# Kernel optimization log

Measured on AMD Instinct MI355X. Metric: run time of the kernel, lower is better.

Reference implementation:

```python
import jax, jax.numpy as jnp
import numpy as np

N_NODES = 10000
N_EDGES = 320000
N_GRAPHS = 64
D_IN = 256
D_HID = 256
D_OUT = 16


def sage_conv(x, edge_index, w_l, b_l, w_r):
    # PyG SAGEConv: out = lin_l(mean_{j in N(i)} x_j) + lin_r(x_i)
    src, dst = edge_index[0], edge_index[1]
    msg = x[src]                                   # [E, d] gather
    summed = jax.ops.segment_sum(msg, dst, num_segments=x.shape[0])
    ones = jnp.ones((edge_index.shape[1],), dtype=x.dtype)
    cnt = jax.ops.segment_sum(ones, dst, num_segments=x.shape[0])
    aggr = summed / jnp.maximum(cnt, 1.0)[:, None]  # mean aggregation
    return aggr @ w_l.T + b_l + x @ w_r.T


def setup_inputs() -> dict:
    key = jax.random.key(0)
    ks = jax.random.split(key, 12)

    def glorot(k, shape):
        lim = float(np.sqrt(6.0 / (shape[0] + shape[1])))
        return jax.random.uniform(k, shape, jnp.float32, -lim, lim)

    x = jax.random.normal(ks[0], (N_NODES, D_IN), jnp.float32)
    edge_index = jax.random.randint(ks[1], (2, N_EDGES), 0, N_NODES, jnp.int64)
    batch = jnp.sort(jax.random.randint(ks[2], (N_NODES,), 0, N_GRAPHS, jnp.int64))

    return {
        "x": x,
        "edge_index": edge_index,
        "batch": batch,
        "w1_l": glorot(ks[3], (D_HID, D_IN)),
        "b1_l": jnp.zeros((D_HID,), jnp.float32),
        "w1_r": glorot(ks[4], (D_HID, D_IN)),
        "w2_l": glorot(ks[5], (D_HID, D_HID)),
        "b2_l": jnp.zeros((D_HID,), jnp.float32),
        "w2_r": glorot(ks[6], (D_HID, D_HID)),
        "w_cls": glorot(ks[7], (D_OUT, D_HID)),
        "b_cls": jnp.zeros((D_OUT,), jnp.float32),
    }


def reference(x, edge_index, batch, w1_l, b1_l, w1_r, w2_l, b2_l, w2_r, w_cls, b_cls):
    h = jax.nn.relu(sage_conv(x, edge_index, w1_l, b1_l, w1_r))
    h = jax.nn.relu(sage_conv(h, edge_index, w2_l, b2_l, w2_r))
    pooled = jax.ops.segment_sum(h, batch, num_segments=N_GRAPHS)  # global_add_pool
    return jax.nn.sigmoid(pooled @ w_cls.T + b_cls)
```

## Files before the change

kernel.cpp:

```cpp
#include <hip/hip_runtime.h>
#include <hip/hip_fp16.h>
#include <math.h>

#define NN 10000
#define NE 320000
#define NG 64
#define DD 256
#define DOUT 16
#define SLOT 96

typedef __attribute__((ext_vector_type(8))) _Float16 f16x8;
typedef __attribute__((ext_vector_type(4))) float f32x4;

#define OFF_CNT   0u
#define OFF_CSR   40064u
#define OFF_XH    3880064u
#define OFF_AGGR  9000064u
#define OFF_H1    14120064u
#define OFF_H2    19240064u
#define OFF_WH    24360064u
#define OFF_POOL  24884352u

__global__ __launch_bounds__(256) void init_kernel(int* __restrict__ cnt,
                                                   float* __restrict__ pooled) {
  int i = blockIdx.x * 256 + threadIdx.x;
  if (i < NN) cnt[i] = 0;
  if (i < NG * DD) pooled[i] = 0.f;
}

#define NFB 1250
#define NXG (NN * DD / 8)
#define NWG 8192
#define NCB ((NXG + 4 * NWG + 255) / 256)
__global__ __launch_bounds__(256) void prep_kernel(
    const int* __restrict__ ei, int* __restrict__ cnt, int* __restrict__ csr,
    const float* __restrict__ x, const float* __restrict__ w1l,
    const float* __restrict__ w1r, const float* __restrict__ w2l,
    const float* __restrict__ w2r, _Float16* __restrict__ xh,
    _Float16* __restrict__ wh) {
  if (blockIdx.x < NFB) {
    int e = blockIdx.x * 256 + threadIdx.x;
    int s = ei[e];
    int d = ei[NE + e];
    int p = atomicAdd(&cnt[d], 1);
    if (p < SLOT) csr[d * SLOT + p] = s;
    return;
  }
  int i = (blockIdx.x - NFB) * 256 + threadIdx.x;
  const float* src;
  _Float16* dst;
  if (i < NXG) {
    src = x + i * 8;
    dst = xh + i * 8;
  } else if (i < NXG + 4 * NWG) {
    int j = i - NXG;
    int w = j >> 13, k = j & (NWG - 1);
    src = ((w == 0) ? w1l : (w == 1) ? w1r : (w == 2) ? w2l : w2r) + k * 8;
    dst = wh + w * 65536 + k * 8;
  } else {
    return;
  }
  const float4* sp = (const float4*)src;
  float4 a = sp[0], b = sp[1];
  f16x8 r;
  r[0] = (_Float16)a.x; r[1] = (_Float16)a.y; r[2] = (_Float16)a.z; r[3] = (_Float16)a.w;
  r[4] = (_Float16)b.x; r[5] = (_Float16)b.y; r[6] = (_Float16)b.z; r[7] = (_Float16)b.w;
  *(f16x8*)dst = r;
}

__global__ __launch_bounds__(256) void aggregate_f16_kernel(
    const _Float16* __restrict__ xin, const int* __restrict__ cnt,
    const int* __restrict__ csr, _Float16* __restrict__ out) {
  const int wave = threadIdx.x >> 6, lane = threadIdx.x & 63;
  const int node = blockIdx.x * 4 + wave;
  if (node >= NN) return;
  const int deg = cnt[node];
  const int n = min(deg, SLOT);
  const int base = node * SLOT;
  const int h = lane >> 5;
  const int cb = (lane & 31) * 8;
  float a[8] = {0.f, 0.f, 0.f, 0.f, 0.f, 0.f, 0.f, 0.f};
  int i = h;
  for (; i + 14 < n; i += 16) {
    f16x8 v[8];
#pragma unroll
    for (int u = 0; u < 8; ++u) {
      int s = csr[base + i + 2 * u];
      v[u] = *(const f16x8*)&xin[s * DD + cb];
    }
#pragma unroll
    for (int j = 0; j < 8; ++j)
      a[j] += (((float)v[0][j] + (float)v[1][j]) + ((float)v[2][j] + (float)v[3][j])) +
              (((float)v[4][j] + (float)v[5][j]) + ((float)v[6][j] + (float)v[7][j]));
  }
  for (; i < n; i += 2) {
    int s = csr[base + i];
    f16x8 v = *(const f16x8*)&xin[s * DD + cb];
#pragma unroll
    for (int j = 0; j < 8; ++j) a[j] += (float)v[j];
  }
#pragma unroll
  for (int j = 0; j < 8; ++j) a[j] += __shfl_xor(a[j], 32);
  if (lane < 32) {
    float inv = 1.0f / fmaxf((float)deg, 1.0f);
    f16x8 r;
#pragma unroll
    for (int j = 0; j < 8; ++j) r[j] = (_Float16)(a[j] * inv);
    *(f16x8*)&out[node * DD + cb] = r;
  }
}

__global__ __launch_bounds__(256) void gemm_mfma_kernel(
    const _Float16* __restrict__ A1, const _Float16* __restrict__ A2,
    const _Float16* __restrict__ W1, const _Float16* __restrict__ W2,
    const float* __restrict__ bias, _Float16* __restrict__ out) {
  __shared__ _Float16 As[2][128][72];
  __shared__ _Float16 Bs[2][64][72];
  const int id = blockIdx.x;
  const int xcd = id & 7;
  const int q = id >> 3;
  const int cblk = q & 3;
  const int rblk = (q >> 2) * 8 + xcd;
  const int row0 = rblk * 128, col0 = cblk * 64;
  if (row0 >= NN) return;

  const int t = threadIdx.x;
  const int lane = t & 63;
  const int wid = t >> 6;
  const int wr = wid >> 1, wc = wid & 1;
  const int sar = t >> 1, sac = (t & 1) * 32;
  const int sbr = t >> 2, sbc = (t & 3) * 16;
  const int fr = lane & 15;
  const int fk = (lane >> 4) * 8;

  int garow = row0 + sar;
  if (garow >= NN) garow = NN - 1;
  const int gbrow = col0 + sbr;

  f32x4 acc[4][2];
#pragma unroll
  for (int m = 0; m < 4; ++m)
#pragma unroll
    for (int n = 0; n < 2; ++n) {
      acc[m][n][0] = 0.f; acc[m][n][1] = 0.f;
      acc[m][n][2] = 0.f; acc[m][n][3] = 0.f;
    }

  f16x8 rA[4], rB[2];

#define LOADSTEP(S)                                                          \
  {                                                                          \
    const _Float16* Ap = ((S) < 4) ? A1 : A2;                                \
    const _Float16* Wp = ((S) < 4) ? W1 : W2;                                \
    const int k0 = ((S) & 3) * 64;                                           \
    _Pragma("unroll") for (int j = 0; j < 4; ++j)                            \
        rA[j] = *(const f16x8*)&Ap[garow * DD + k0 + sac + 8 * j];           \
    _Pragma("unroll") for (int j = 0; j < 2; ++j)                            \
        rB[j] = *(const f16x8*)&Wp[gbrow * DD + k0 + sbc + 8 * j];           \
  }

#define WRITESTEP(B)                                                         \
  {                                                                          \
    _Pragma("unroll") for (int j = 0; j < 4; ++j)                            \
        *(f16x8*)&As[B][sar][sac + 8 * j] = rA[j];                           \
    _Pragma("unroll") for (int j = 0; j < 2; ++j)                            \
        *(f16x8*)&Bs[B][sbr][sbc + 8 * j] = rB[j];                           \
  }

  LOADSTEP(0);
  WRITESTEP(0);
  LOADSTEP(1);
  __syncthreads();

#pragma unroll
  for (int s = 0; s < 8; ++s) {
    const int b = s & 1;
#pragma unroll
    for (int kk = 0; kk < 2; ++kk) {
      f16x8 af[4], bf[2];
#pragma unroll
      for (int m = 0; m < 4; ++m)
        af[m] = *(const f16x8*)&As[b][wr * 64 + m * 16 + fr][kk * 32 + fk];
#pragma unroll
      for (int n = 0; n < 2; ++n)
        bf[n] = *(const f16x8*)&Bs[b][wc * 32 + n * 16 + fr][kk * 32 + fk];
#pragma unroll
      for (int m = 0; m < 4; ++m)
#pragma unroll
        for (int n = 0; n < 2; ++n)
          acc[m][n] = __builtin_amdgcn_mfma_f32_16x16x32_f16(af[m], bf[n], acc[m][n], 0, 0, 0);
    }
    if (s < 7) {
      WRITESTEP(1 - b);
      if (s < 6) LOADSTEP(s + 2);
      __syncthreads();
    }
  }
#undef LOADSTEP
#undef WRITESTEP

  const int orow = row0 + wr * 64 + (lane >> 4) * 4;
  const int ocol = col0 + wc * 32 + fr;
#pragma unroll
  for (int m = 0; m < 4; ++m)
#pragma unroll
    for (int n = 0; n < 2; ++n) {
      int col = ocol + n * 16;
      float bv = bias[col];
#pragma unroll
      for (int j = 0; j < 4; ++j) {
        int row = orow + m * 16 + j;
        if (row < NN) {
          float v = acc[m][n][j] + bv;
          out[row * DD + col] = (_Float16)fmaxf(v, 0.f);
        }
      }
    }
}

__global__ __launch_bounds__(256) void pool_chunk_kernel(const _Float16* __restrict__ h2,
                                                         const int* __restrict__ batch,
                                                         float* __restrict__ pooled) {
  const int c = threadIdx.x;
  const int n0 = blockIdx.x * 16;
  const int n1 = min(n0 + 16, NN);
  if (n0 >= NN) return;
  float acc = 0.f;
  int g = batch[n0];
  for (int i = n0; i < n1; ++i) {
    int gi = batch[i];
    if (gi != g) {
      atomicAdd(&pooled[g * DD + c], acc);
      acc = 0.f;
      g = gi;
    }
    acc += (float)h2[i * DD + c];
  }
  atomicAdd(&pooled[g * DD + c], acc);
}

__global__ __launch_bounds__(256) void cls_kernel(const float* __restrict__ pooled,
                                                  const float* __restrict__ wc,
                                                  const float* __restrict__ bc,
                                                  float* __restrict__ out) {
  int t = blockIdx.x * 256 + threadIdx.x;
  if (t >= NG * DOUT) return;
  int g = t >> 4, j = t & 15;
  float s = bc[j];
  for (int k = 0; k < DD; k += 4) {
    float4 p = *(const float4*)&pooled[g * DD + k];
    float4 w = *(const float4*)&wc[j * DD + k];
    s += p.x * w.x + p.y * w.y + p.z * w.z + p.w * w.w;
  }
  out[t] = 1.0f / (1.0f + expf(-s));
}

extern "C" void kernel_launch(void* const* d_in, const int* in_sizes, int n_in,
                              void* d_out, int out_size, void* d_ws, size_t ws_size,
                              hipStream_t stream) {
  const float* x     = (const float*)d_in[0];
  const int*   ei    = (const int*)d_in[1];
  const int*   batch = (const int*)d_in[2];
  const float* w1_l  = (const float*)d_in[3];
  const float* b1_l  = (const float*)d_in[4];
  const float* w1_r  = (const float*)d_in[5];
  const float* w2_l  = (const float*)d_in[6];
  const float* b2_l  = (const float*)d_in[7];
  const float* w2_r  = (const float*)d_in[8];
  const float* w_cls = (const float*)d_in[9];
  const float* b_cls = (const float*)d_in[10];
  float* out = (float*)d_out;

  char* ws = (char*)d_ws;
  int*       cnt    = (int*)(ws + OFF_CNT);
  int*       csr    = (int*)(ws + OFF_CSR);
  _Float16*  xh     = (_Float16*)(ws + OFF_XH);
  _Float16*  aggr   = (_Float16*)(ws + OFF_AGGR);
  _Float16*  h1     = (_Float16*)(ws + OFF_H1);
  _Float16*  h2     = (_Float16*)(ws + OFF_H2);
  _Float16*  wh     = (_Float16*)(ws + OFF_WH);
  float*     pooled = (float*)(ws + OFF_POOL);

  init_kernel<<<64, 256, 0, stream>>>(cnt, pooled);

  prep_kernel<<<NFB + NCB, 256, 0, stream>>>(ei, cnt, csr, x, w1_l, w1_r,
                                             w2_l, w2_r, xh, wh);

  aggregate_f16_kernel<<<(NN + 3) / 4, 256, 0, stream>>>(xh, cnt, csr, aggr);
  gemm_mfma_kernel<<<320, 256, 0, stream>>>(aggr, xh, wh, wh + 65536, b1_l, h1);

  aggregate_f16_kernel<<<(NN + 3) / 4, 256, 0, stream>>>(h1, cnt, csr, aggr);
  gemm_mfma_kernel<<<320, 256, 0, stream>>>(aggr, h1, wh + 2 * 65536, wh + 3 * 65536, b2_l, h2);

  pool_chunk_kernel<<<(NN + 15) / 16, 256, 0, stream>>>(h2, batch, pooled);
  cls_kernel<<<4, 256, 0, stream>>>(pooled, w_cls, b_cls, out);
}
```

Before: 110.7 us.

## Split neighbor aggregation into two column-half passes for cache locality

Each aggregation is split into two launches, each covering 128 of the 256 feature columns. Within a pass, every wave handles one node with four 16-lane groups, each taking a strided subset of the edges, and the partial sums are combined with two shuffle reductions. The aim is to halve the gathered working set per pass so more of the source feature matrix stays in L2/MALL, and the output uses nontemporal stores. In exchange the CSR indices are read twice, there are extra kernel launches, and each load is 16 bytes from a 256-byte half-row.

```diff
diff --git a/kernel.cpp b/kernel.cpp
--- a/kernel.cpp
+++ b/kernel.cpp
@@ -68,45 +68,50 @@
   *(f16x8*)dst = r;
 }
 
-__global__ __launch_bounds__(256) void aggregate_f16_kernel(
+__global__ __launch_bounds__(256) void aggregate_half_kernel(
     const _Float16* __restrict__ xin, const int* __restrict__ cnt,
-    const int* __restrict__ csr, _Float16* __restrict__ out) {
+    const int* __restrict__ csr, _Float16* __restrict__ out, int chbase) {
   const int wave = threadIdx.x >> 6, lane = threadIdx.x & 63;
   const int node = blockIdx.x * 4 + wave;
   if (node >= NN) return;
   const int deg = cnt[node];
   const int n = min(deg, SLOT);
   const int base = node * SLOT;
-  const int h = lane >> 5;
-  const int cb = (lane & 31) * 8;
+  const int q = lane >> 4;
+  const int cb = chbase + (lane & 15) * 8;
   float a[8] = {0.f, 0.f, 0.f, 0.f, 0.f, 0.f, 0.f, 0.f};
-  int i = h;
-  for (; i + 14 < n; i += 16) {
-    f16x8 v[8];
-#pragma unroll
-    for (int u = 0; u < 8; ++u) {
-      int s = csr[base + i + 2 * u];
-      v[u] = *(const f16x8*)&xin[s * DD + cb];
-    }
+  int i = q;
+  for (; i + 12 < n; i += 16) {
+    f16x8 v0 = *(const f16x8*)&xin[csr[base + i     ] * DD + cb];
+    f16x8 v1 = *(const f16x8*)&xin[csr[base + i + 4 ] * DD + cb];
+    f16x8 v2 = *(const f16x8*)&xin[csr[base + i + 8 ] * DD + cb];
+    f16x8 v3 = *(const f16x8*)&xin[csr[base + i + 12] * DD + cb];
 #pragma unroll
     for (int j = 0; j < 8; ++j)
-      a[j] += (((float)v[0][j] + (float)v[1][j]) + ((float)v[2][j] + (float)v[3][j])) +
-              (((float)v[4][j] + (float)v[5][j]) + ((float)v[6][j] + (float)v[7][j]));
-  }
-  for (; i < n; i += 2) {
-    int s = csr[base + i];
-    f16x8 v = *(const f16x8*)&xin[s * DD + cb];
+      a[j] += ((float)v0[j] + (float)v1[j]) + ((float)v2[j] + (float)v3[j]);
+  }
+  for (; i + 4 < n; i += 8) {
+    f16x8 v0 = *(const f16x8*)&xin[csr[base + i    ] * DD + cb];
+    f16x8 v1 = *(const f16x8*)&xin[csr[base + i + 4] * DD + cb];
+#pragma unroll
+    for (int j = 0; j < 8; ++j) a[j] += (float)v0[j] + (float)v1[j];
+  }
+  for (; i < n; i += 4) {
+    f16x8 v = *(const f16x8*)&xin[csr[base + i] * DD + cb];
 #pragma unroll
     for (int j = 0; j < 8; ++j) a[j] += (float)v[j];
   }
 #pragma unroll
-  for (int j = 0; j < 8; ++j) a[j] += __shfl_xor(a[j], 32);
-  if (lane < 32) {
+  for (int j = 0; j < 8; ++j) {
+    a[j] += __shfl_xor(a[j], 16);
+    a[j] += __shfl_xor(a[j], 32);
+  }
+  if (lane < 16) {
     float inv = 1.0f / fmaxf((float)deg, 1.0f);
     f16x8 r;
 #pragma unroll
     for (int j = 0; j < 8; ++j) r[j] = (_Float16)(a[j] * inv);
-    *(f16x8*)&out[node * DD + cb] = r;
+    __builtin_nontemporal_store(r, (f16x8*)&out[node * DD + cb]);
   }
 }
 
@@ -286,10 +291,14 @@
   prep_kernel<<<NFB + NCB, 256, 0, stream>>>(ei, cnt, csr, x, w1_l, w1_r,
                                              w2_l, w2_r, xh, wh);
 
-  aggregate_f16_kernel<<<(NN + 3) / 4, 256, 0, stream>>>(xh, cnt, csr, aggr);
+  const int agrid = (NN + 3) / 4;
+
+  aggregate_half_kernel<<<agrid, 256, 0, stream>>>(xh, cnt, csr, aggr, 0);
+  aggregate_half_kernel<<<agrid, 256, 0, stream>>>(xh, cnt, csr, aggr, 128);
   gemm_mfma_kernel<<<320, 256, 0, stream>>>(aggr, xh, wh, wh + 65536, b1_l, h1);
 
-  aggregate_f16_kernel<<<(NN + 3) / 4, 256, 0, stream>>>(h1, cnt, csr, aggr);
+  aggregate_half_kernel<<<agrid, 256, 0, stream>>>(h1, cnt, csr, aggr, 0);
+  aggregate_half_kernel<<<agrid, 256, 0, stream>>>(h1, cnt, csr, aggr, 128);
   gemm_mfma_kernel<<<320, 256, 0, stream>>>(aggr, h1, wh + 2 * 65536, wh + 3 * 65536, b2_l, h2);
 
   pool_chunk_kernel<<<(NN + 15) / 16, 256, 0, stream>>>(h2, batch, pooled);
```

Result: slower. 113.9 us (+2.9%).

## Use direct global-to-LDS loads with XOR swizzle in GEMM; fuse pool and classifier

Applied to the files above, without the earlier changes.

The GEMM tile staging now uses global_load_lds to copy A and B tiles straight into an XOR-swizzled LDS layout, issuing the next stage before the MFMA loop. This removes the register round-trip and the padded layout. Separately, the pooling kernel now does the classifier itself: a last-block-done atomic counter lets the final block compute the sigmoid outputs, which removes one kernel launch. The risks are whether the LDS lane-to-address mapping is correct and the cost of the fences in every pool block.

```diff
diff --git a/kernel.cpp b/kernel.cpp
--- a/kernel.cpp
+++ b/kernel.cpp
@@ -20,12 +20,21 @@
 #define OFF_H2    19240064u
 #define OFF_WH    24360064u
 #define OFF_POOL  24884352u
+#define OFF_DONE  24949888u
+
+__device__ __forceinline__ void gload16(const void* g, void* l) {
+  __builtin_amdgcn_global_load_lds(
+      (const __attribute__((address_space(1))) void*)g,
+      (__attribute__((address_space(3))) void*)l, 16, 0, 0);
+}
 
 __global__ __launch_bounds__(256) void init_kernel(int* __restrict__ cnt,
-                                                   float* __restrict__ pooled) {
+                                                   float* __restrict__ pooled,
+                                                   int* __restrict__ done) {
   int i = blockIdx.x * 256 + threadIdx.x;
   if (i < NN) cnt[i] = 0;
   if (i < NG * DD) pooled[i] = 0.f;
+  if (i == 0) *done = 0;
 }
 
 #define NFB 1250
@@ -114,8 +123,8 @@
     const _Float16* __restrict__ A1, const _Float16* __restrict__ A2,
     const _Float16* __restrict__ W1, const _Float16* __restrict__ W2,
     const float* __restrict__ bias, _Float16* __restrict__ out) {
-  __shared__ _Float16 As[2][128][72];
-  __shared__ _Float16 Bs[2][64][72];
+  __shared__ _Float16 As[2][128 * 64];
+  __shared__ _Float16 Bs[2][64 * 64];
   const int id = blockIdx.x;
   const int xcd = id & 7;
   const int q = id >> 3;
@@ -128,14 +137,10 @@
   const int lane = t & 63;
   const int wid = t >> 6;
   const int wr = wid >> 1, wc = wid & 1;
-  const int sar = t >> 1, sac = (t & 1) * 32;
-  const int sbr = t >> 2, sbc = (t & 3) * 16;
   const int fr = lane & 15;
-  const int fk = (lane >> 4) * 8;
-
-  int garow = row0 + sar;
-  if (garow >= NN) garow = NN - 1;
-  const int gbrow = col0 + sbr;
+  const int fg = lane >> 4;
+  const int srl = lane >> 3;
+  const int cj = lane & 7;
 
   f32x4 acc[4][2];
 #pragma unroll
@@ -146,58 +151,56 @@
       acc[m][n][2] = 0.f; acc[m][n][3] = 0.f;
     }
 
-  f16x8 rA[4], rB[2];
-
-#define LOADSTEP(S)                                                          \
-  {                                                                          \
-    const _Float16* Ap = ((S) < 4) ? A1 : A2;                                \
-    const _Float16* Wp = ((S) < 4) ? W1 : W2;                                \
-    const int k0 = ((S) & 3) * 64;                                           \
-    _Pragma("unroll") for (int j = 0; j < 4; ++j)                            \
-        rA[j] = *(const f16x8*)&Ap[garow * DD + k0 + sac + 8 * j];           \
-    _Pragma("unroll") for (int j = 0; j < 2; ++j)                            \
-        rB[j] = *(const f16x8*)&Wp[gbrow * DD + k0 + sbc + 8 * j];           \
-  }
-
-#define WRITESTEP(B)                                                         \
-  {                                                                          \
-    _Pragma("unroll") for (int j = 0; j < 4; ++j)                            \
-        *(f16x8*)&As[B][sar][sac + 8 * j] = rA[j];                           \
-    _Pragma("unroll") for (int j = 0; j < 2; ++j)                            \
-        *(f16x8*)&Bs[B][sbr][sbc + 8 * j] = rB[j];                           \
-  }
-
-  LOADSTEP(0);
-  WRITESTEP(0);
-  LOADSTEP(1);
+#define STAGE(B, S)                                                           \
+  {                                                                           \
+    const _Float16* Ap = ((S) < 4) ? A1 : A2;                                 \
+    const _Float16* Wp = ((S) < 4) ? W1 : W2;                                 \
+    const int k0 = ((S) & 3) * 64;                                            \
+    _Pragma("unroll") for (int j = 0; j < 4; ++j) {                           \
+      int row = (wid * 4 + j) * 8 + srl;                          \
+      int gr = row0 + row; if (gr >= NN) gr = NN - 1;                         \
+      int gc = cj ^ (row & 7);                                                \
+      gload16(Ap + (size_t)gr * DD + k0 + gc * 8, &As[B][(wid * 4 + j) * 512]);\
+    }                                                                         \
+    _Pragma("unroll") for (int j = 0; j < 2; ++j) {                           \
+      int row = (wid * 2 + j) * 8 + srl;                           \
+      int gc = cj ^ (row & 7);                                                \
+      gload16(Wp + (size_t)(col0 + row) * DD + k0 + gc * 8,                   \
+              &Bs[B][(wid * 2 + j) * 512]);                                   \
+    }                                                                         \
+  }
+
+  STAGE(0, 0);
   __syncthreads();
 
 #pragma unroll
   for (int s = 0; s < 8; ++s) {
     const int b = s & 1;
+    if (s < 7) STAGE(1 - b, s + 1);
 #pragma unroll
     for (int kk = 0; kk < 2; ++kk) {
       f16x8 af[4], bf[2];
 #pragma unroll
-      for (int m = 0; m < 4; ++m)
-        af[m] = *(const f16x8*)&As[b][wr * 64 + m * 16 + fr][kk * 32 + fk];
-#pragma unroll
-      for (int n = 0; n < 2; ++n)
-        bf[n] = *(const f16x8*)&Bs[b][wc * 32 + n * 16 + fr][kk * 32 + fk];
+      for (int m = 0; m < 4; ++m) {
+        int row = wr * 64 + m * 16 + fr;
+        int ch = (kk * 4 + fg) ^ (row & 7);
+        af[m] = *(const f16x8*)&As[b][row * 64 + ch * 8];
+      }
+#pragma unroll
+      for (int n = 0; n < 2; ++n) {
+        int row = wc * 32 + n * 16 + fr;
+        int ch = (kk * 4 + fg) ^ (row & 7);
+        bf[n] = *(const f16x8*)&Bs[b][row * 64 + ch * 8];
+      }
 #pragma unroll
       for (int m = 0; m < 4; ++m)
 #pragma unroll
         for (int n = 0; n < 2; ++n)
           acc[m][n] = __builtin_amdgcn_mfma_f32_16x16x32_f16(af[m], bf[n], acc[m][n], 0, 0, 0);
     }
-    if (s < 7) {
-      WRITESTEP(1 - b);
-      if (s < 6) LOADSTEP(s + 2);
-      __syncthreads();
-    }
-  }
-#undef LOADSTEP
-#undef WRITESTEP
+    __syncthreads();
+  }
+#undef STAGE
 
   const int orow = row0 + wr * 64 + (lane >> 4) * 4;
   const int ocol = col0 + wc * 32 + fr;
@@ -218,16 +221,16 @@
     }
 }
 
-__global__ __launch_bounds__(256) void pool_chunk_kernel(const _Float16* __restrict__ h2,
-                                                         const int* __restrict__ batch,
-                                                         float* __restrict__ pooled) {
+__global__ __launch_bounds__(256) void pool_cls_kernel(
+    const _Float16* __restrict__ h2, const int* __restrict__ batch,
+    float* __restrict__ pooled, const float* __restrict__ wc,
+    const float* __restrict__ bc, float* __restrict__ out,
+    int* __restrict__ done) {
   const int c = threadIdx.x;
   const int n0 = blockIdx.x * 16;
-  const int n1 = min(n0 + 16, NN);
-  if (n0 >= NN) return;
   float acc = 0.f;
   int g = batch[n0];
-  for (int i = n0; i < n1; ++i) {
+  for (int i = n0; i < n0 + 16; ++i) {
     int gi = batch[i];
     if (gi != g) {
       atomicAdd(&pooled[g * DD + c], acc);
@@ -237,22 +240,38 @@
     acc += (float)h2[i * DD + c];
   }
   atomicAdd(&pooled[g * DD + c], acc);
-}
-
-__global__ __launch_bounds__(256) void cls_kernel(const float* __restrict__ pooled,
-                                                  const float* __restrict__ wc,
-                                                  const float* __restrict__ bc,
-                                                  float* __restrict__ out) {
-  int t = blockIdx.x * 256 + threadIdx.x;
-  if (t >= NG * DOUT) return;
-  int g = t >> 4, j = t & 15;
-  float s = bc[j];
+
+  __shared__ int last;
+  __syncthreads();
+  __threadfence();
+  if (c == 0) {
+    int v = __hip_atomic_fetch_add(done, 1, __ATOMIC_ACQ_REL, __HIP_MEMORY_SCOPE_AGENT);
+    last = (v == (int)gridDim.x - 1) ? 1 : 0;
+  }
+  __syncthreads();
+  if (!last) return;
+
+  const int gg = c >> 2;
+  const int j0 = (c & 3) * 4;
+  float s0 = bc[j0], s1 = bc[j0 + 1], s2 = bc[j0 + 2], s3 = bc[j0 + 3];
   for (int k = 0; k < DD; k += 4) {
-    float4 p = *(const float4*)&pooled[g * DD + k];
-    float4 w = *(const float4*)&wc[j * DD + k];
-    s += p.x * w.x + p.y * w.y + p.z * w.z + p.w * w.w;
-  }
-  out[t] = 1.0f / (1.0f + expf(-s));
+    float p0 = __hip_atomic_load(&pooled[gg * DD + k + 0], __ATOMIC_RELAXED, __HIP_MEMORY_SCOPE_AGENT);
+    float p1 = __hip_atomic_load(&pooled[gg * DD + k + 1], __ATOMIC_RELAXED, __HIP_MEMORY_SCOPE_AGENT);
+    float p2 = __hip_atomic_load(&pooled[gg * DD + k + 2], __ATOMIC_RELAXED, __HIP_MEMORY_SCOPE_AGENT);
+    float p3 = __hip_atomic_load(&pooled[gg * DD + k + 3], __ATOMIC_RELAXED, __HIP_MEMORY_SCOPE_AGENT);
+    float4 w0 = *(const float4*)&wc[(j0 + 0) * DD + k];
+    float4 w1 = *(const float4*)&wc[(j0 + 1) * DD + k];
+    float4 w2 = *(const float4*)&wc[(j0 + 2) * DD + k];
+    float4 w3 = *(const float4*)&wc[(j0 + 3) * DD + k];
+    s0 += p0 * w0.x + p1 * w0.y + p2 * w0.z + p3 * w0.w;
+    s1 += p0 * w1.x + p1 * w1.y + p2 * w1.z + p3 * w1.w;
+    s2 += p0 * w2.x + p1 * w2.y + p2 * w2.z + p3 * w2.w;
+    s3 += p0 * w3.x + p1 * w3.y + p2 * w3.z + p3 * w3.w;
+  }
+  out[gg * DOUT + j0 + 0] = 1.f / (1.f + expf(-s0));
+  out[gg * DOUT + j0 + 1] = 1.f / (1.f + expf(-s1));
+  out[gg * DOUT + j0 + 2] = 1.f / (1.f + expf(-s2));
+  out[gg * DOUT + j0 + 3] = 1.f / (1.f + expf(-s3));
 }
 
 extern "C" void kernel_launch(void* const* d_in, const int* in_sizes, int n_in,
@@ -280,18 +299,21 @@
   _Float16*  h2     = (_Float16*)(ws + OFF_H2);
   _Float16*  wh     = (_Float16*)(ws + OFF_WH);
   float*     pooled = (float*)(ws + OFF_POOL);
-
-  init_kernel<<<64, 256, 0, stream>>>(cnt, pooled);
+  int*       done   = (int*)(ws + OFF_DONE);
+
+  init_kernel<<<64, 256, 0, stream>>>(cnt, pooled, done);
 
   prep_kernel<<<NFB + NCB, 256, 0, stream>>>(ei, cnt, csr, x, w1_l, w1_r,
                                              w2_l, w2_r, xh, wh);
 
-  aggregate_f16_kernel<<<(NN + 3) / 4, 256, 0, stream>>>(xh, cnt, csr, aggr);
+  const int agrid = (NN + 3) / 4;
+
+  aggregate_f16_kernel<<<agrid, 256, 0, stream>>>(xh, cnt, csr, aggr);
   gemm_mfma_kernel<<<320, 256, 0, stream>>>(aggr, xh, wh, wh + 65536, b1_l, h1);
 
-  aggregate_f16_kernel<<<(NN + 3) / 4, 256, 0, stream>>>(h1, cnt, csr, aggr);
+  aggregate_f16_kernel<<<agrid, 256, 0, stream>>>(h1, cnt, csr, aggr);
   gemm_mfma_kernel<<<320, 256, 0, stream>>>(aggr, h1, wh + 2 * 65536, wh + 3 * 65536, b2_l, h2);
 
-  pool_chunk_kernel<<<(NN + 15) / 16, 256, 0, stream>>>(h2, batch, pooled);
-  cls_kernel<<<4, 256, 0, stream>>>(pooled, w_cls, b_cls, out);
-}
+  pool_cls_kernel<<<(NN + 15) / 16, 256, 0, stream>>>(h2, batch, pooled,
+                                                      w_cls, b_cls, out, done);
+}
```

New measurement: 182.9 us. +65.2%, slower.
